# Kernel optimization log

Hardware: AMD Instinct MI355X
Metric: run time of the kernel (lower is better)

## Reference

```python
import jax, jax.numpy as jnp
import numpy as np

VOCAB, HID = 32000, 1024
SEQ, BATCH = 64, 32

def setup_inputs() -> dict:
    key = jax.random.key(0)
    ks = jax.random.split(key, 12)
    w = 0.1  # winit uniform(-winit, winit)
    u = lambda k, shape: jax.random.uniform(k, shape, jnp.float32, -w, w)
    return {
        "x": jax.random.randint(ks[0], (SEQ, BATCH), 0, VOCAB),
        "emb_W": u(ks[1], (VOCAB, HID)),
        "Wx0": u(ks[2], (4 * HID, HID)), "Wh0": u(ks[3], (4 * HID, HID)),
        "bx0": u(ks[4], (4 * HID,)), "bh0": u(ks[5], (4 * HID,)),
        "Wx1": u(ks[6], (4 * HID, HID)), "Wh1": u(ks[7], (4 * HID, HID)),
        "bx1": u(ks[8], (4 * HID,)), "bh1": u(ks[9], (4 * HID,)),
        "fc_W": u(ks[10], (VOCAB, HID)), "fc_b": u(ks[11], (VOCAB,)),
        "h0": jnp.zeros((BATCH, HID), jnp.float32),
        "c0": jnp.zeros((BATCH, HID), jnp.float32),
        "h1": jnp.zeros((BATCH, HID), jnp.float32),
        "c1": jnp.zeros((BATCH, HID), jnp.float32),
    }

def _lstm_layer(inp, h, c, Wx, Wh, bx, bh):
    # inp: [T, B, H]; h, c: [B, H]
    def step(carry, x_t):
        h, c = carry
        gx = x_t @ Wx.T + bx      # [B, 4H]
        gh = h @ Wh.T + bh        # [B, 4H]
        xi, xf, xo, xn = jnp.split(gx, 4, axis=1)
        hi, hf, ho, hn = jnp.split(gh, 4, axis=1)
        i = jax.nn.sigmoid(xi + hi)
        f = jax.nn.sigmoid(xf + hf)
        o = jax.nn.sigmoid(xo + ho)
        n = jnp.tanh(xn + hn)
        c = f * c + i * n
        h = o * jnp.tanh(c)
        return (h, c), h
    (h, c), ys = jax.lax.scan(step, (h, c), inp)
    return ys, h, c

def reference(x, emb_W, Wx0, Wh0, bx0, bh0, Wx1, Wh1, bx1, bh1,
              fc_W, fc_b, h0, c0, h1, c1):
    e = emb_W[x]                                   # [T, B, H] embedding gather
    y0, h0f, c0f = _lstm_layer(e, h0, c0, Wx0, Wh0, bx0, bh0)
    y1, h1f, c1f = _lstm_layer(y0, h1, c1, Wx1, Wh1, bx1, bh1)
    # Linear.forward flattens to [T*B, H] then projects to vocab (dropout=0)
    logits = y1.reshape(-1, y1.shape[-1]) @ fc_W.T + fc_b  # [T*B, V]
    return logits, h0f, c0f, h1f, c1f
```

## Files before the change

kernel.cpp:

```cpp
#include <hip/hip_runtime.h>
#include <hip/hip_bf16.h>
#include <stdint.h>

typedef __bf16 bf16x8 __attribute__((ext_vector_type(8)));
typedef float  f32x4  __attribute__((ext_vector_type(4)));

#define HID   1024
#define SEQT  64
#define BATCH 32
#define GATES 4096
#define ROWS  2048
#define VOCAB 32000
#define HSLAB (64 * 32 * 16)
#define AGT __HIP_MEMORY_SCOPE_AGENT

__device__ __forceinline__ unsigned short f2bf(float f) {
    union { float f; unsigned u; } v; v.f = f;
    unsigned u = v.u + 0x7FFFu + ((v.u >> 16) & 1u);
    return (unsigned short)(u >> 16);
}

__device__ __forceinline__ float sigm(float x) { return 1.f / (1.f + expf(-x)); }

__device__ __forceinline__ void gload_lds16(const void* g, void* l) {
    __builtin_amdgcn_global_load_lds(
        (const __attribute__((address_space(1))) unsigned int*)g,
        (__attribute__((address_space(3))) unsigned int*)l,
        16, 0, 0);
}

__device__ __forceinline__ ushort4 cvt4(float4 v) {
    ushort4 o;
    o.x = f2bf(v.x); o.y = f2bf(v.y); o.z = f2bf(v.z); o.w = f2bf(v.w);
    return o;
}

__global__ __launch_bounds__(256) void prologue_k(
    const int* __restrict__ x, const float* __restrict__ embW,
    unsigned short* __restrict__ eb,
    const float* __restrict__ Wx0, unsigned short* __restrict__ Wx0b,
    const float* __restrict__ h0, const float* __restrict__ h1,
    unsigned short* __restrict__ h0b, unsigned short* __restrict__ h1b,
    int* __restrict__ bar)
{
    const int bid = blockIdx.x, tid = threadIdx.x;
    const float4* src = (const float4*)(embW + (size_t)x[bid] * HID);
    ((ushort4*)(eb + (size_t)bid * HID))[tid] = cvt4(src[tid]);
    int base = bid * 512 + tid;
    ((ushort4*)Wx0b)[base]       = cvt4(((const float4*)Wx0)[base]);
    ((ushort4*)Wx0b)[base + 256] = cvt4(((const float4*)Wx0)[base + 256]);
    int i = bid * 256 + tid;
    if (i < 32768) {
        int blk = i >> 9, b = (i >> 4) & 31, w = i & 15;
        int col = blk * 16 + w;
        h0b[i] = f2bf(h0[b * HID + col]);
        h1b[i] = f2bf(h1[b * HID + col]);
        if (i < 8192) bar[i] = 0;
    }
}

__global__ __launch_bounds__(512) void gemm_bt(
    const unsigned short* __restrict__ A,
    const unsigned short* __restrict__ B,
    float* __restrict__ C,
    const float* __restrict__ bias0,
    const float* __restrict__ bias1)
{
    __shared__ unsigned short As[256 * 64];
    __shared__ unsigned short Bs[128 * 64];
    const int tid  = threadIdx.x;
    const int lane = tid & 63;
    const int wave = tid >> 6;
    const int wr   = wave >> 1;
    const int wc   = wave & 1;
    const int lr   = lane & 15;
    const int lk2  = (lane >> 4) * 16;

    const int per = 256 >> 3;
    const int wid = ((int)blockIdx.x & 7) * per + ((int)blockIdx.x >> 3);
    const int bm  = (wid & 7) << 8;
    const int bn  = (wid >> 3) << 7;

    f32x4 acc[4][4];
    #pragma unroll
    for (int m = 0; m < 4; ++m)
        #pragma unroll
        for (int n = 0; n < 4; ++n) acc[m][n] = 0.f;

    for (int kt = 0; kt < HID; kt += 64) {
        __syncthreads();
        #pragma unroll
        for (int i = 0; i < 4; ++i) {
            int ch = tid + i * 512;
            int row = ch >> 3, ck = ch & 7;
            int e = kt + ((ck ^ (row & 7)) << 3);
            gload_lds16(A + (size_t)(bm + row) * HID + e, (char*)As + ch * 16);
        }
        #pragma unroll
        for (int i = 0; i < 2; ++i) {
            int ch = tid + i * 512;
            int row = ch >> 3, ck = ch & 7;
            int e = kt + ((ck ^ (row & 7)) << 3);
            gload_lds16(B + (size_t)(bn + row) * HID + e, (char*)Bs + ch * 16);
        }
        __syncthreads();
        #pragma unroll
        for (int kh = 0; kh < 2; ++kh) {
            bf16x8 af[4], bfr[4];
            #pragma unroll
            for (int m = 0; m < 4; ++m) {
                int row = wr * 64 + m * 16 + lr;
                af[m] = *(const bf16x8*)((char*)As + row * 128 +
                         ((kh * 64 + lk2) ^ ((row & 7) << 4)));
            }
            #pragma unroll
            for (int n = 0; n < 4; ++n) {
                int row = wc * 64 + n * 16 + lr;
                bfr[n] = *(const bf16x8*)((char*)Bs + row * 128 +
                         ((kh * 64 + lk2) ^ ((row & 7) << 4)));
            }
            #pragma unroll
            for (int m = 0; m < 4; ++m)
                #pragma unroll
                for (int n = 0; n < 4; ++n)
                    acc[m][n] = __builtin_amdgcn_mfma_f32_16x16x32_bf16(
                        af[m], bfr[n], acc[m][n], 0, 0, 0);
        }
    }

    const int row0 = bm + wr * 64, col0 = bn + wc * 64;
    #pragma unroll
    for (int n = 0; n < 4; ++n) {
        int col = col0 + n * 16 + lr;
        float badd = bias0[col] + bias1[col];
        #pragma unroll
        for (int m = 0; m < 4; ++m) {
            #pragma unroll
            for (int j = 0; j < 4; ++j) {
                int row = row0 + m * 16 + (lane >> 4) * 4 + j;
                C[(size_t)row * GATES + col] = acc[m][n][j] + badd;
            }
        }
    }
}

__global__ __launch_bounds__(256, 1) void lstm_fused_k(
    const float* __restrict__ Wh0f,
    const float* __restrict__ Wx1f,
    const float* __restrict__ Wh1f,
    const float* __restrict__ gx0,
    const float* __restrict__ bx1,
    const float* __restrict__ bh1,
    const unsigned short* __restrict__ h0b,
    const unsigned short* __restrict__ h1b,
    const float* __restrict__ c0i,
    const float* __restrict__ c1i,
    unsigned short* __restrict__ y0x,
    unsigned short* __restrict__ y1x,
    float* __restrict__ part,
    float* __restrict__ h0f, float* __restrict__ c0f,
    float* __restrict__ h1f, float* __restrict__ c1f,
    int* __restrict__ bar,
    const float* __restrict__ fcW,
    unsigned short* __restrict__ fcWb)
{
    const int tid  = threadIdx.x;
    const int bid  = blockIdx.x;
    const int xcd  = bid & 7;
    const int role = xcd >> 1;
    const int wg   = ((bid >> 3) << 1) | (xcd & 1);

    if (role == 3) {
        int base = wg * 256 + tid;
        const float4* f4 = (const float4*)fcW;
        uint4* o4 = (uint4*)fcWb;
        const int n8 = VOCAB * HID / 8;
        for (int i = base; i < n8; i += 16384) {
            float4 v0 = f4[2 * i], v1 = f4[2 * i + 1];
            uint4 o;
            o.x = (unsigned)f2bf(v0.x) | ((unsigned)f2bf(v0.y) << 16);
            o.y = (unsigned)f2bf(v0.z) | ((unsigned)f2bf(v0.w) << 16);
            o.z = (unsigned)f2bf(v1.x) | ((unsigned)f2bf(v1.y) << 16);
            o.w = (unsigned)f2bf(v1.z) | ((unsigned)f2bf(v1.w) << 16);
            o4[i] = o;
        }
        return;
    }

    __builtin_amdgcn_fence(__ATOMIC_ACQUIRE, "agent");

    __shared__ char smem[65536 + 8192];
    float* pre = (float*)(smem + 65536);
    const int lane = tid & 63;
    const int wave = tid >> 6;
    const int lr   = lane & 15;
    const int lk8  = (lane >> 4) * 8;
    const int r0   = lr, r1 = 16 + lr;
    const int kby  = (lane >> 4) * 16;
    const int eb_  = tid >> 3;
    const int ecp  = (tid & 7) * 2;
    const int ecol = wg * 16 + ecp;

    bf16x8 wf[32];
    {
        const float* Wsrc = (role == 0) ? Wh0f : (role == 1) ? Wx1f : Wh1f;
        const float* p = Wsrc + (size_t)(wave * HID + wg * 16 + lr) * HID + lk8;
        #pragma unroll
        for (int kk = 0; kk < 32; ++kk) {
            float4 v0 = *(const float4*)(p + kk * 32);
            float4 v1 = *(const float4*)(p + kk * 32 + 4);
            union { bf16x8 v; unsigned short s[8]; } u;
            u.s[0] = f2bf(v0.x); u.s[1] = f2bf(v0.y);
            u.s[2] = f2bf(v0.z); u.s[3] = f2bf(v0.w);
            u.s[4] = f2bf(v1.x); u.s[5] = f2bf(v1.y);
            u.s[6] = f2bf(v1.z); u.s[7] = f2bf(v1.w);
            wf[kk] = u.v;
        }
        #pragma unroll
        for (int kk = 0; kk < 32; ++kk) asm volatile("" : "+v"(wf[kk]));
    }

    auto stage_g = [&](const unsigned short* src) {
        #pragma unroll
        for (int j = 0; j < 16; ++j) {
            int base = wave * 16384 + j * 1024;
            int d = base + lane * 16;
            int r = d >> 11;
            int cb = (d & 2047) ^ ((r & 7) << 4);
            int e0 = cb >> 1;
            int g = (((e0 >> 4) * 32 + r) * 16 + (e0 & 15)) * 2;
            gload_lds16((const char*)src + g, smem + base);
        }
    };
    auto mm = [&](f32x4& A0, f32x4& A1) {
        #pragma unroll
        for (int kk = 0; kk < 32; ++kk) {
            int k2 = kk * 64 + kby;
            bf16x8 x0 = *(const bf16x8*)(smem + r0 * 2048 + (k2 ^ ((r0 & 7) << 4)));
            bf16x8 x1 = *(const bf16x8*)(smem + r1 * 2048 + (k2 ^ ((r1 & 7) << 4)));
            A0 = __builtin_amdgcn_mfma_f32_16x16x32_bf16(x0, wf[kk], A0, 0, 0, 0);
            A1 = __builtin_amdgcn_mfma_f32_16x16x32_bf16(x1, wf[kk], A1, 0, 0, 0);
        }
    };
    auto spill = [&](const f32x4& a0, const f32x4& a1) {
        float* pg = pre + wave * 512;
        #pragma unroll
        for (int j = 0; j < 4; ++j) {
            pg[((lane >> 4) * 4 + j) * 16 + lr]        = a0[j];
            pg[((lane >> 4) * 4 + j + 16) * 16 + lr]   = a1[j];
        }
    };
    auto pollge = [&](int grp, int val) {
        for (;;) {
            int f = __hip_atomic_load(&bar[(grp * 64 + lane) * 32],
                                      __ATOMIC_RELAXED, AGT);
            if (__all(f >= val)) break;
            __builtin_amdgcn_s_sleep(1);
        }
    };

    if (role == 0) {
        float creg0, creg1;
        { float2 c2 = *(const float2*)&c0i[eb_ * HID + ecol]; creg0 = c2.x; creg1 = c2.y; }
        for (int t = 0; t < SEQT; ++t) {
            float2 gpre[4];
            const float* gxr = gx0 + (size_t)(t * BATCH + eb_) * GATES + ecol;
            #pragma unroll
            for (int g = 0; g < 4; ++g) gpre[g] = *(const float2*)(gxr + g * HID);
            if (t > 0) pollge(0, t);
            asm volatile("" ::: "memory");
            stage_g(t == 0 ? h0b : y0x + (size_t)(t - 1) * HSLAB);
            __syncthreads();
            f32x4 a0 = 0.f, a1 = 0.f;
            mm(a0, a1);
            spill(a0, a1);
            __syncthreads();
            float2 P[4];
            #pragma unroll
            for (int g = 0; g < 4; ++g) {
                float2 pr = *(const float2*)&pre[(g * 32 + eb_) * 16 + ecp];
                P[g].x = pr.x + gpre[g].x; P[g].y = pr.y + gpre[g].y;
            }
            float i0 = sigm(P[0].x), fg0 = sigm(P[1].x), o0 = sigm(P[2].x), n0 = tanhf(P[3].x);
            float i1 = sigm(P[0].y), fg1 = sigm(P[1].y), o1 = sigm(P[2].y), n1 = tanhf(P[3].y);
            float cn0 = fg0 * creg0 + i0 * n0, cn1 = fg1 * creg1 + i1 * n1;
            float hv0 = o0 * tanhf(cn0), hv1 = o1 * tanhf(cn1);
            creg0 = cn0; creg1 = cn1;
            unsigned pk = (unsigned)f2bf(hv0) | ((unsigned)f2bf(hv1) << 16);
            __hip_atomic_store(
                (unsigned*)&y0x[(size_t)t * HSLAB + (wg * 32 + eb_) * 16 + ecp],
                pk, __ATOMIC_RELAXED, AGT);
            if (t == SEQT - 1) {
                *(float2*)&h0f[eb_ * HID + ecol] = make_float2(hv0, hv1);
                *(float2*)&c0f[eb_ * HID + ecol] = make_float2(cn0, cn1);
            }
            __syncthreads();
            if (tid == 0)
                __hip_atomic_store(&bar[wg * 32], t + 1, __ATOMIC_RELAXED, AGT);
        }
    } else if (role == 1) {
        for (int t = 0; t < SEQT; ++t) {
            pollge(0, t + 1);
            asm volatile("" ::: "memory");
            stage_g(y0x + (size_t)t * HSLAB);
            __syncthreads();
            f32x4 a0 = 0.f, a1 = 0.f;
            mm(a0, a1);
            {
                float* pb = part + (((size_t)(t * 4 + wave) * 64 + wg) * 32) * 16;
                int brow = (lane >> 4) * 4;
                #pragma unroll
                for (int j = 0; j < 4; ++j) {
                    __hip_atomic_store(pb + (brow + j) * 16 + lr,      a0[j],
                                       __ATOMIC_RELAXED, AGT);
                    __hip_atomic_store(pb + (brow + j + 16) * 16 + lr, a1[j],
                                       __ATOMIC_RELAXED, AGT);
                }
            }
            __syncthreads();
            if (tid == 0)
                __hip_atomic_store(&bar[(64 + wg) * 32], t + 1, __ATOMIC_RELAXED, AGT);
        }
    } else {
        float creg0, creg1;
        { float2 c2 = *(const float2*)&c1i[eb_ * HID + ecol]; creg0 = c2.x; creg1 = c2.y; }
        float2 b1r[4];
        #pragma unroll
        for (int g = 0; g < 4; ++g) {
            float2 a = *(const float2*)&bx1[g * HID + ecol];
            float2 b = *(const float2*)&bh1[g * HID + ecol];
            b1r[g].x = a.x + b.x; b1r[g].y = a.y + b.y;
        }
        for (int t = 0; t < SEQT; ++t) {
            pollge(1, t + 1);
            if (t > 0) pollge(2, t);
            asm volatile("" ::: "memory");
            stage_g(t == 0 ? h1b : y1x + (size_t)(t - 1) * HSLAB);
            __syncthreads();
            f32x4 a0 = 0.f, a1 = 0.f;
            mm(a0, a1);
            spill(a0, a1);
            __syncthreads();
            float2 P[4];
            #pragma unroll
            for (int g = 0; g < 4; ++g) {
                float2 pr = *(const float2*)&pre[(g * 32 + eb_) * 16 + ecp];
                float2 px = *(const float2*)(part +
                    ((((size_t)(t * 4 + g) * 64 + wg) * 32 + eb_) * 16 + ecp));
                P[g].x = pr.x + px.x + b1r[g].x;
                P[g].y = pr.y + px.y + b1r[g].y;
            }
            float i0 = sigm(P[0].x), fg0 = sigm(P[1].x), o0 = sigm(P[2].x), n0 = tanhf(P[3].x);
            float i1 = sigm(P[0].y), fg1 = sigm(P[1].y), o1 = sigm(P[2].y), n1 = tanhf(P[3].y);
            float cn0 = fg0 * creg0 + i0 * n0, cn1 = fg1 * creg1 + i1 * n1;
            float hv0 = o0 * tanhf(cn0), hv1 = o1 * tanhf(cn1);
            creg0 = cn0; creg1 = cn1;
            unsigned pk = (unsigned)f2bf(hv0) | ((unsigned)f2bf(hv1) << 16);
            __hip_atomic_store(
                (unsigned*)&y1x[(size_t)t * HSLAB + (wg * 32 + eb_) * 16 + ecp],
                pk, __ATOMIC_RELAXED, AGT);
            if (t == SEQT - 1) {
                *(float2*)&h1f[eb_ * HID + ecol] = make_float2(hv0, hv1);
                *(float2*)&c1f[eb_ * HID + ecol] = make_float2(cn0, cn1);
            }
            __syncthreads();
            if (tid == 0)
                __hip_atomic_store(&bar[(128 + wg) * 32], t + 1, __ATOMIC_RELAXED, AGT);
        }
    }
}

__global__ __launch_bounds__(512) void fc_k(
    const unsigned short* __restrict__ y1x,
    const unsigned short* __restrict__ fcWb,
    const float* __restrict__ fcb,
    float* __restrict__ logits)
{
    __shared__ unsigned short As[256 * 64];
    __shared__ unsigned short Bs[128 * 64];
    const int tid  = threadIdx.x;
    const int lane = tid & 63;
    const int wave = tid >> 6;
    const int wr   = wave >> 1;
    const int wc   = wave & 1;
    const int lr   = lane & 15;
    const int lk2  = (lane >> 4) * 16;

    const int per = 2000 >> 3;
    const int wid = ((int)blockIdx.x & 7) * per + ((int)blockIdx.x >> 3);
    const int bm  = (wid & 7) << 8;
    const int bn  = (wid >> 3) << 7;

    f32x4 acc[4][4];
    #pragma unroll
    for (int m = 0; m < 4; ++m)
        #pragma unroll
        for (int n = 0; n < 4; ++n) acc[m][n] = 0.f;

    for (int kt = 0; kt < HID; kt += 64) {
        __syncthreads();
        #pragma unroll
        for (int i = 0; i < 4; ++i) {
            int ch = tid + i * 512;
            int row = ch >> 3, ck = ch & 7;
            int R = bm + row;
            int e = kt + ((ck ^ (row & 7)) << 3);
            const char* asrc = (const char*)y1x +
                ((((size_t)(R >> 5) * 64 + (e >> 4)) * 32 + (R & 31)) * 16 + (e & 15)) * 2;
            gload_lds16(asrc, (char*)As + ch * 16);
        }
        #pragma unroll
        for (int i = 0; i < 2; ++i) {
            int ch = tid + i * 512;
            int row = ch >> 3, ck = ch & 7;
            int e = kt + ((ck ^ (row & 7)) << 3);
            gload_lds16(fcWb + (size_t)(bn + row) * HID + e, (char*)Bs + ch * 16);
        }
        __syncthreads();
        #pragma unroll
        for (int kh = 0; kh < 2; ++kh) {
            bf16x8 af[4], bfr[4];
            #pragma unroll
            for (int m = 0; m < 4; ++m) {
                int row = wr * 64 + m * 16 + lr;
                af[m] = *(const bf16x8*)((char*)As + row * 128 +
                         ((kh * 64 + lk2) ^ ((row & 7) << 4)));
            }
            #pragma unroll
            for (int n = 0; n < 4; ++n) {
                int row = wc * 64 + n * 16 + lr;
                bfr[n] = *(const bf16x8*)((char*)Bs + row * 128 +
                         ((kh * 64 + lk2) ^ ((row & 7) << 4)));
            }
            #pragma unroll
            for (int m = 0; m < 4; ++m)
                #pragma unroll
                for (int n = 0; n < 4; ++n)
                    acc[m][n] = __builtin_amdgcn_mfma_f32_16x16x32_bf16(
                        af[m], bfr[n], acc[m][n], 0, 0, 0);
        }
    }

    const int row0 = bm + wr * 64, col0 = bn + wc * 64;
    #pragma unroll
    for (int n = 0; n < 4; ++n) {
        int col = col0 + n * 16 + lr;
        float badd = fcb[col];
        #pragma unroll
        for (int m = 0; m < 4; ++m) {
            #pragma unroll
            for (int j = 0; j < 4; ++j) {
                int row = row0 + m * 16 + (lane >> 4) * 4 + j;
                logits[(size_t)row * VOCAB + col] = acc[m][n][j] + badd;
            }
        }
    }
}

extern "C" void kernel_launch(void* const* d_in, const int* in_sizes, int n_in,
                              void* d_out, int out_size, void* d_ws, size_t ws_size,
                              hipStream_t stream) {
    const int*   x    = (const int*)d_in[0];
    const float* embW = (const float*)d_in[1];
    const float* Wx0  = (const float*)d_in[2];
    const float* Wh0  = (const float*)d_in[3];
    const float* bx0  = (const float*)d_in[4];
    const float* bh0  = (const float*)d_in[5];
    const float* Wx1  = (const float*)d_in[6];
    const float* Wh1  = (const float*)d_in[7];
    const float* bx1  = (const float*)d_in[8];
    const float* bh1  = (const float*)d_in[9];
    const float* fcW  = (const float*)d_in[10];
    const float* fcb  = (const float*)d_in[11];
    const float* h0   = (const float*)d_in[12];
    const float* c0   = (const float*)d_in[13];
    const float* h1   = (const float*)d_in[14];
    const float* c1   = (const float*)d_in[15];

    char* ws = (char*)d_ws;
    size_t off = 0;
    auto alloc = [&](size_t bytes) {
        char* p = ws + off;
        off += (bytes + 255) & ~(size_t)255;
        return p;
    };
    unsigned short* eb    = (unsigned short*)alloc((size_t)ROWS * HID * 2);
    unsigned short* Wx0b  = (unsigned short*)alloc((size_t)GATES * HID * 2);
    unsigned short* fcWb  = (unsigned short*)alloc((size_t)VOCAB * HID * 2);
    float*          gx0   = (float*)alloc((size_t)ROWS * GATES * 4);
    float*          part  = (float*)alloc((size_t)SEQT * 4 * 64 * 32 * 16 * 4);
    unsigned short* y0x   = (unsigned short*)alloc((size_t)SEQT * HSLAB * 2);
    unsigned short* y1x   = (unsigned short*)alloc((size_t)SEQT * HSLAB * 2);
    unsigned short* h0b   = (unsigned short*)alloc((size_t)BATCH * HID * 2);
    unsigned short* h1b   = (unsigned short*)alloc((size_t)BATCH * HID * 2);
    int*            bar   = (int*)alloc((size_t)256 * 32 * 4);
    (void)ws_size; (void)in_sizes; (void)n_in; (void)out_size;

    float* logits = (float*)d_out;
    float* h0f = logits + (size_t)ROWS * VOCAB;
    float* c0f = h0f + BATCH * HID;
    float* h1f = c0f + BATCH * HID;
    float* c1f = h1f + BATCH * HID;

    prologue_k<<<ROWS, 256, 0, stream>>>(x, embW, eb, Wx0, Wx0b,
                                         h0, h1, h0b, h1b, bar);
    gemm_bt<<<256, 512, 0, stream>>>(eb, Wx0b, gx0, bx0, bh0);
    lstm_fused_k<<<256, 256, 0, stream>>>(Wh0, Wx1, Wh1, gx0, bx1, bh1,
                                          h0b, h1b, c0, c1, y0x, y1x, part,
                                          h0f, c0f, h1f, c1f, bar, fcW, fcWb);
    fc_k<<<2000, 512, 0, stream>>>(y1x, fcWb, fcb, logits);
}
```

Baseline: 539.0 us.

## Double-buffer FC GEMM with 256x256 tiles and interleaved async LDS staging

Rewrites the vocab projection GEMM to use 256x256 block tiles (1000 blocks instead of 2000), double-buffered LDS (128KB), and async global-to-LDS loads for the next K tile interleaved with MFMA groups. It also raises wave priority around the MFMA bursts. The aim is to hide global load latency and halve redundant operand traffic per output. The costs are heavier register pressure (32 accumulators per lane) and 128KB of LDS, which limits occupancy to one block per CU.

Result: no change. 529.9 us (-1.7%).

```diff
diff --git a/kernel.cpp b/kernel.cpp
--- a/kernel.cpp
+++ b/kernel.cpp
@@ -28,6 +28,8 @@
         (__attribute__((address_space(3))) unsigned int*)l,
         16, 0, 0);
 }
+
+#define MBAR() asm volatile("s_barrier" ::: "memory")
 
 __device__ __forceinline__ ushort4 cvt4(float4 v) {
     ushort4 o;
@@ -376,78 +378,115 @@
     const float* __restrict__ fcb,
     float* __restrict__ logits)
 {
-    __shared__ unsigned short As[256 * 64];
-    __shared__ unsigned short Bs[128 * 64];
+    __shared__ char smem[131072];
     const int tid  = threadIdx.x;
     const int lane = tid & 63;
     const int wave = tid >> 6;
-    const int wr   = wave >> 1;
-    const int wc   = wave & 1;
+    const int wr   = wave >> 2;
+    const int wc   = wave & 3;
     const int lr   = lane & 15;
     const int lk2  = (lane >> 4) * 16;
 
-    const int per = 2000 >> 3;
-    const int wid = ((int)blockIdx.x & 7) * per + ((int)blockIdx.x >> 3);
-    const int bm  = (wid & 7) << 8;
-    const int bn  = (wid >> 3) << 7;
-
-    f32x4 acc[4][4];
-    #pragma unroll
-    for (int m = 0; m < 4; ++m)
-        #pragma unroll
-        for (int n = 0; n < 4; ++n) acc[m][n] = 0.f;
-
-    for (int kt = 0; kt < HID; kt += 64) {
-        __syncthreads();
-        #pragma unroll
-        for (int i = 0; i < 4; ++i) {
-            int ch = tid + i * 512;
-            int row = ch >> 3, ck = ch & 7;
-            int R = bm + row;
-            int e = kt + ((ck ^ (row & 7)) << 3);
-            const char* asrc = (const char*)y1x +
-                ((((size_t)(R >> 5) * 64 + (e >> 4)) * 32 + (R & 31)) * 16 + (e & 15)) * 2;
-            gload_lds16(asrc, (char*)As + ch * 16);
-        }
+    const int chunk = (int)blockIdx.x >> 3;
+    const int wid   = ((int)blockIdx.x & 7) * 125 + chunk;
+    const int bm    = (wid % 8) << 8;
+    const int bn    = (wid / 8) << 8;
+
+    auto stage_half = [&](int hh, int kt, int buf) {
         #pragma unroll
         for (int i = 0; i < 2; ++i) {
             int ch = tid + i * 512;
             int row = ch >> 3, ck = ch & 7;
-            int e = kt + ((ck ^ (row & 7)) << 3);
-            gload_lds16(fcWb + (size_t)(bn + row) * HID + e, (char*)Bs + ch * 16);
-        }
-        __syncthreads();
-        #pragma unroll
-        for (int kh = 0; kh < 2; ++kh) {
-            bf16x8 af[4], bfr[4];
-            #pragma unroll
-            for (int m = 0; m < 4; ++m) {
-                int row = wr * 64 + m * 16 + lr;
-                af[m] = *(const bf16x8*)((char*)As + row * 128 +
-                         ((kh * 64 + lk2) ^ ((row & 7) << 4)));
-            }
-            #pragma unroll
-            for (int n = 0; n < 4; ++n) {
-                int row = wc * 64 + n * 16 + lr;
-                bfr[n] = *(const bf16x8*)((char*)Bs + row * 128 +
-                         ((kh * 64 + lk2) ^ ((row & 7) << 4)));
-            }
-            #pragma unroll
-            for (int m = 0; m < 4; ++m)
+            int e = kt * 64 + ((ck ^ (row & 7)) << 3);
+            if (hh < 2) {
+                char* dst = smem + buf * 32768 + hh * 16384 + ch * 16;
+                int R = bm + hh * 128 + row;
+                const char* src = (const char*)y1x +
+                    ((((size_t)(R >> 5) * 64 + (e >> 4)) * 32 + (R & 31)) * 16 + (e & 15)) * 2;
+                gload_lds16(src, dst);
+            } else {
+                char* dst = smem + 65536 + buf * 32768 + (hh - 2) * 16384 + ch * 16;
+                int R = bn + (hh - 2) * 128 + row;
+                gload_lds16(fcWb + (size_t)R * HID + e, dst);
+            }
+        }
+    };
+
+    f32x4 acc[8][4];
+    #pragma unroll
+    for (int m = 0; m < 8; ++m)
+        #pragma unroll
+        for (int n = 0; n < 4; ++n) acc[m][n] = 0.f;
+
+    bf16x8 bfr[4][2];
+    auto ldb = [&](int buf) {
+        const char* Bb = smem + 65536 + buf * 32768 + (wc >> 1) * 16384;
+        #pragma unroll
+        for (int n = 0; n < 4; ++n)
+            #pragma unroll
+            for (int kh = 0; kh < 2; ++kh) {
+                int rB = (wc & 1) * 64 + n * 16 + lr;
+                bfr[n][kh] = *(const bf16x8*)(Bb + rB * 128 +
+                              ((kh * 64 + lk2) ^ ((rB & 7) << 4)));
+            }
+    };
+    auto mgrp = [&](int buf, int g) {
+        const char* Ab = smem + buf * 32768 + wr * 16384;
+        bf16x8 af[2][2];
+        #pragma unroll
+        for (int mi = 0; mi < 2; ++mi)
+            #pragma unroll
+            for (int kh = 0; kh < 2; ++kh) {
+                int rA = (g * 2 + mi) * 16 + lr;
+                af[mi][kh] = *(const bf16x8*)(Ab + rA * 128 +
+                              ((kh * 64 + lk2) ^ ((rA & 7) << 4)));
+            }
+        __builtin_amdgcn_s_setprio(1);
+        #pragma unroll
+        for (int mi = 0; mi < 2; ++mi)
+            #pragma unroll
+            for (int n = 0; n < 4; ++n)
                 #pragma unroll
-                for (int n = 0; n < 4; ++n)
-                    acc[m][n] = __builtin_amdgcn_mfma_f32_16x16x32_bf16(
-                        af[m], bfr[n], acc[m][n], 0, 0, 0);
-        }
-    }
-
-    const int row0 = bm + wr * 64, col0 = bn + wc * 64;
+                for (int kh = 0; kh < 2; ++kh)
+                    acc[g * 2 + mi][n] = __builtin_amdgcn_mfma_f32_16x16x32_bf16(
+                        af[mi][kh], bfr[n][kh], acc[g * 2 + mi][n], 0, 0, 0);
+        __builtin_amdgcn_s_setprio(0);
+    };
+
+    stage_half(0, 0, 0); stage_half(1, 0, 0);
+    stage_half(2, 0, 0); stage_half(3, 0, 0);
+
+    int cbuf = 0;
+    for (int kt = 0; kt < 15; ++kt) {
+        MBAR();
+        stage_half(0, kt + 1, cbuf ^ 1);
+        asm volatile("s_waitcnt vmcnt(2)" ::: "memory");
+        __builtin_amdgcn_sched_barrier(0);
+        MBAR();
+        ldb(cbuf);
+        stage_half(1, kt + 1, cbuf ^ 1);
+        mgrp(cbuf, 0);
+        stage_half(2, kt + 1, cbuf ^ 1);
+        mgrp(cbuf, 1);
+        stage_half(3, kt + 1, cbuf ^ 1);
+        mgrp(cbuf, 2);
+        mgrp(cbuf, 3);
+        cbuf ^= 1;
+    }
+    MBAR();
+    asm volatile("s_waitcnt vmcnt(0)" ::: "memory");
+    __builtin_amdgcn_sched_barrier(0);
+    MBAR();
+    ldb(cbuf);
+    mgrp(cbuf, 0); mgrp(cbuf, 1); mgrp(cbuf, 2); mgrp(cbuf, 3);
+
+    const int row0 = bm + wr * 128, col0 = bn + wc * 64;
     #pragma unroll
     for (int n = 0; n < 4; ++n) {
         int col = col0 + n * 16 + lr;
         float badd = fcb[col];
         #pragma unroll
-        for (int m = 0; m < 4; ++m) {
+        for (int m = 0; m < 8; ++m) {
             #pragma unroll
             for (int j = 0; j < 4; ++j) {
                 int row = row0 + m * 16 + (lane >> 4) * 4 + j;
@@ -508,5 +547,5 @@
     lstm_fused_k<<<256, 256, 0, stream>>>(Wh0, Wx1, Wh1, gx0, bx1, bh1,
                                           h0b, h1b, c0, c1, y0x, y1x, part,
                                           h0f, c0f, h1f, c1f, bar, fcW, fcWb);
-    fc_k<<<2000, 512, 0, stream>>>(y1x, fcWb, fcb, logits);
-}
+    fc_k<<<1000, 512, 0, stream>>>(y1x, fcWb, fcb, logits);
+}
```
